# Optimization experiments

Measured on AMD Instinct MI355X. Metric: run time of the kernel, lower is better.

Reference implementation:

```python
import jax, jax.numpy as jnp
import numpy as np

B, S, D, H = 1, 2048, 1024, 16
HD = D // H
S_SLOPE = 10.0      # soft_thres_layer s
C_MASK = -10000.0   # soft_thres_layer c == masked_bias
ALPHA = 0.0         # config.threshold
W_STD = 0.02        # GPT2 init std for weights


def setup_inputs() -> dict:
    key = jax.random.key(0)
    k1, k2, k3 = jax.random.split(key, 3)
    return {
        "hidden_states": jax.random.normal(k1, (B, S, D), dtype=jnp.float32),
        "c_attn_w": jax.random.normal(k2, (D, 3 * D), dtype=jnp.float32) * W_STD,
        "c_attn_b": jnp.zeros((3 * D,), dtype=jnp.float32),
        "c_proj_w": jax.random.normal(k3, (D, D), dtype=jnp.float32) * W_STD,
        "c_proj_b": jnp.zeros((D,), dtype=jnp.float32),
    }


def reference(hidden_states, c_attn_w, c_attn_b, c_proj_w, c_proj_b):
    # Conv1D: x @ w + b (GPT2 convention: weight is [in, out])
    qkv = hidden_states @ c_attn_w + c_attn_b            # [B,S,3D]
    q, k, v = jnp.split(qkv, 3, axis=-1)

    def split_heads(x):
        return x.reshape(B, S, H, HD).transpose(0, 2, 1, 3)  # [B,H,S,hd]

    q, k, v = split_heads(q), split_heads(k), split_heads(v)

    # prun path: NO 1/sqrt(d) scaling (skipped when self.prun is True)
    w = jnp.einsum("bhqd,bhkd->bhqk", q, k)              # [B,H,S,S]

    causal = jnp.tril(jnp.ones((S, S), dtype=bool))[None, None]
    w = jnp.where(causal, w, C_MASK)

    # soft-threshold pruning: smoothly pushes scores below alpha toward c=-10000
    w = C_MASK + (w - C_MASK) * jax.nn.sigmoid(S_SLOPE * (w - ALPHA))

    a = jax.nn.softmax(w, axis=-1)                        # attn_dropout = identity (eval)
    out = jnp.einsum("bhqk,bhkd->bhqd", a, v)             # [B,H,S,hd]
    out = out.transpose(0, 2, 1, 3).reshape(B, S, D)      # merge heads
    return out @ c_proj_w + c_proj_b                      # resid_dropout = identity
```

## Files before the change

kernel.cpp:

```cpp
#include <hip/hip_runtime.h>


#define S_LEN 2048
#define DM    1024
#define NH    16
#define HD    64
#define NQKV  3072
#define SLOPE 10.0f
#define CMASK -10000.0f

typedef short s16x4 __attribute__((ext_vector_type(4)));
typedef short s16x8 __attribute__((ext_vector_type(8)));
typedef float f32x4 __attribute__((ext_vector_type(4)));

#define MFMA16(a,b,c) __builtin_amdgcn_mfma_f32_16x16x32_bf16(a,b,c,0,0,0)
#define GLDS16(g,l) __builtin_amdgcn_global_load_lds( \
    (const __attribute__((address_space(1))) void*)(g), \
    (__attribute__((address_space(3))) void*)(l), 16, 0, 0)

__device__ __forceinline__ short f2bf(float f){
    unsigned u = __float_as_uint(f);
    u += 0x7fffu + ((u >> 16) & 1u);
    return (short)(u >> 16);
}
__device__ __forceinline__ float bf2f(short x){
    return __uint_as_float(((unsigned)(unsigned short)x) << 16);
}
struct bfpair { short hi, lo; };
__device__ __forceinline__ bfpair split_bf(float x){
    bfpair r; r.hi = f2bf(x);
    r.lo = f2bf(x - bf2f(r.hi));
    return r;
}

template<int ROWS, int THREADS>
__device__ __forceinline__ void stage_tile(const short* gbase, int rstride,
                                           short* lds, int tid){
#pragma unroll
    for (int it = 0; it < ROWS*8/THREADS; ++it){
        int s = it*THREADS + tid;
        int row = s >> 3, grp = s & 7;
        const short* src = gbase + (size_t)row*rstride + ((grp ^ (row & 7)) << 3);
        GLDS16(src, lds + (size_t)s*8);
    }
}
__device__ __forceinline__ s16x8 frag(const short* lds, int row, int kg){
    return *(const s16x8*)&lds[row*64 + ((kg ^ (row & 7)) << 3)];
}

template<bool WSPLIT, bool QKV>
__global__ __launch_bounds__(256)
void gemm_kern(const short* __restrict__ Ahg, const short* __restrict__ Alg,
               const short* __restrict__ Bhg, const short* __restrict__ Blg,
               const float* __restrict__ bias,
               short* __restrict__ o0h, short* __restrict__ o0l,
               short* __restrict__ o1h,
               short* __restrict__ o2,  float* __restrict__ oproj)
{
    __shared__ __align__(16) short Ah_s[128*64];
    __shared__ __align__(16) short Al_s[128*64];
    __shared__ __align__(16) short Bh_s[128*64];
    __shared__ __align__(16) short Bl_s[WSPLIT ? 128*64 : 8];

    const int tid = threadIdx.x, lane = tid & 63, wid = tid >> 6;
    const int lr = lane & 15, lg = lane >> 4;
    const int brow = blockIdx.y*128, bcol = blockIdx.x*128;
    const int wm = (wid >> 1)*64, wn = (wid & 1)*64;

    f32x4 acc[4][4];
#pragma unroll
    for (int m = 0; m < 4; ++m)
#pragma unroll
        for (int n = 0; n < 4; ++n) acc[m][n] = (f32x4){0.f,0.f,0.f,0.f};

    for (int k0 = 0; k0 < DM; k0 += 64){
        stage_tile<128,256>(Ahg + (size_t)brow*DM + k0, DM, Ah_s, tid);
        stage_tile<128,256>(Alg + (size_t)brow*DM + k0, DM, Al_s, tid);
        stage_tile<128,256>(Bhg + (size_t)bcol*DM + k0, DM, Bh_s, tid);
        if constexpr (WSPLIT)
            stage_tile<128,256>(Blg + (size_t)bcol*DM + k0, DM, Bl_s, tid);
        __syncthreads();
#pragma unroll
        for (int kc = 0; kc < 2; ++kc){
            s16x8 ah[4], al[4], bh[4], bl[4];
#pragma unroll
            for (int m = 0; m < 4; ++m){
                ah[m] = frag(Ah_s, wm + m*16 + lr, kc*4 + lg);
                al[m] = frag(Al_s, wm + m*16 + lr, kc*4 + lg);
            }
#pragma unroll
            for (int n = 0; n < 4; ++n){
                bh[n] = frag(Bh_s, wn + n*16 + lr, kc*4 + lg);
                if constexpr (WSPLIT)
                    bl[n] = frag(Bl_s, wn + n*16 + lr, kc*4 + lg);
            }
#pragma unroll
            for (int m = 0; m < 4; ++m)
#pragma unroll
                for (int n = 0; n < 4; ++n){
                    acc[m][n] = MFMA16(ah[m], bh[n], acc[m][n]);
                    if constexpr (WSPLIT)
                        acc[m][n] = MFMA16(ah[m], bl[n], acc[m][n]);
                    acc[m][n] = MFMA16(al[m], bh[n], acc[m][n]);
                }
        }
        __syncthreads();
    }

    const int sec = bcol >> 10;
#pragma unroll
    for (int m = 0; m < 4; ++m)
#pragma unroll
        for (int n = 0; n < 4; ++n){
            int row  = brow + wm + m*16 + lg*4;
            int gcol = bcol + wn + n*16 + lr;
            float bv = bias[gcol];
#pragma unroll
            for (int v = 0; v < 4; ++v){
                float val = acc[m][n][v] + bv;
                if constexpr (QKV){
                    int col1 = gcol & 1023;
                    size_t o = (size_t)(row + v)*DM + col1;
                    if (sec == 0){ bfpair p = split_bf(val); o0h[o] = p.hi; o0l[o] = p.lo; }
                    else if (sec == 1){ o1h[o] = f2bf(val); }
                    else { o2[o] = f2bf(val); }
                } else {
                    oproj[(size_t)(row + v)*DM + gcol] = val;
                }
            }
        }
}

__global__ __launch_bounds__(256)
void split_f32(const float* __restrict__ x, short* __restrict__ h,
               short* __restrict__ l, int n4)
{
    int i = blockIdx.x*256 + threadIdx.x;
    if (i >= n4) return;
    float4 v = *(const float4*)&x[(size_t)i*4];
    bfpair a = split_bf(v.x), b = split_bf(v.y), c = split_bf(v.z), d = split_bf(v.w);
    s16x4 hv, lv;
    hv.x = a.hi; hv.y = b.hi; hv.z = c.hi; hv.w = d.hi;
    lv.x = a.lo; lv.y = b.lo; lv.z = c.lo; lv.w = d.lo;
    *(s16x4*)&h[(size_t)i*4] = hv;
    *(s16x4*)&l[(size_t)i*4] = lv;
}

template<bool SPL>
__global__ __launch_bounds__(256)
void wtrans(const float* __restrict__ W, int N, short* __restrict__ Th,
            short* __restrict__ Tl)
{
    __shared__ float t[64][65];
    const int tid = threadIdx.x;
    const int tn = blockIdx.x*64, tk = blockIdx.y*64;
#pragma unroll
    for (int it = 0; it < 4; ++it){
        int idx = tid + it*256;
        int r = idx >> 4, c4 = (idx & 15)*4;
        float4 v = *(const float4*)&W[(size_t)(tk + r)*N + tn + c4];
        t[r][c4] = v.x; t[r][c4+1] = v.y; t[r][c4+2] = v.z; t[r][c4+3] = v.w;
    }
    __syncthreads();
#pragma unroll
    for (int it = 0; it < 4; ++it){
        int idx = tid + it*256;
        int n = idx >> 4, c4 = (idx & 15)*4;
        s16x4 hv, lv;
#pragma unroll
        for (int j = 0; j < 4; ++j){
            bfpair p = split_bf(t[c4+j][n]);
            hv[j] = p.hi; lv[j] = p.lo;
        }
        *(s16x4*)&Th[(size_t)(tn + n)*DM + tk + c4] = hv;
        if constexpr (SPL) *(s16x4*)&Tl[(size_t)(tn + n)*DM + tk + c4] = lv;
    }
}

__global__ __launch_bounds__(256)
void vtrans(const short* __restrict__ Vb, short* __restrict__ Vt)
{
    __shared__ short t[64][66];
    const int tid = threadIdx.x;
    const int td = blockIdx.x*64, ts = blockIdx.y*64;
#pragma unroll
    for (int it = 0; it < 4; ++it){
        int idx = tid + it*256;
        int r = idx >> 4, c4 = (idx & 15)*4;
        s16x4 v = *(const s16x4*)&Vb[(size_t)(ts + r)*DM + td + c4];
        t[r][c4] = v.x; t[r][c4+1] = v.y; t[r][c4+2] = v.z; t[r][c4+3] = v.w;
    }
    __syncthreads();
#pragma unroll
    for (int it = 0; it < 4; ++it){
        int idx = tid + it*256;
        int n = idx >> 4, c4 = (idx & 15)*4;
        s16x4 o;
#pragma unroll
        for (int j = 0; j < 4; ++j) o[j] = t[c4+j][n];
        *(s16x4*)&Vt[(size_t)(td + n)*S_LEN + ts + c4] = o;
    }
}

__global__ __launch_bounds__(64)
void sv_partial(const short* __restrict__ Vb, float* __restrict__ PB)
{
    int b = blockIdx.x, h = blockIdx.y, d = threadIdx.x;
    float s = 0.f;
#pragma unroll 8
    for (int k = 0; k < 64; ++k)
        s += bf2f(Vb[(size_t)(b*64 + k)*DM + h*HD + d]);
    PB[((size_t)h*32 + b)*64 + d] = s;
}
__global__ __launch_bounds__(64)
void sv_suffix(const float* __restrict__ PB, float* __restrict__ SSV)
{
    int h = blockIdx.x, d = threadIdx.x;
    float s = 0.f;
    SSV[((size_t)h*33 + 32)*64 + d] = 0.f;
    for (int b = 31; b >= 0; --b){
        s += PB[((size_t)h*32 + b)*64 + d];
        SSV[((size_t)h*33 + b)*64 + d] = s;
    }
}

__global__ __launch_bounds__(64)
void attn_fwd(const short* __restrict__ Qh, const short* __restrict__ Ql,
              const short* __restrict__ Kh, const short* __restrict__ Vt,
              const float* __restrict__ SSV,
              short* __restrict__ Oh, short* __restrict__ Ol)
{
    __shared__ __align__(16) short Ps[16*72];

    const int id = blockIdx.x;
    const int h  = (id & 7) + 8*((id >> 3) & 1);
    const int qt = 127 - (id >> 4);
    const int diag = qt >> 2;

    const int lane = threadIdx.x, lr = lane & 15, lg = lane >> 4;
    const int qrow = qt*16 + lg*4;

    const short* qbh = Qh + (size_t)(qt*16)*DM + h*HD;
    const short* qbl = Ql + (size_t)(qt*16)*DM + h*HD;
    s16x8 aqh[2], aql[2];
#pragma unroll
    for (int kc = 0; kc < 2; ++kc){
        aqh[kc] = *(const s16x8*)&qbh[(size_t)lr*DM + kc*32 + lg*8];
        aql[kc] = *(const s16x8*)&qbl[(size_t)lr*DM + kc*32 + lg*8];
    }

    float m_run[4], l_run[4];
    f32x4 acc_o[4];
#pragma unroll
    for (int v = 0; v < 4; ++v){ m_run[v] = -1e30f; l_run[v] = 0.f; }
#pragma unroll
    for (int n = 0; n < 4; ++n) acc_o[n] = (f32x4){0.f,0.f,0.f,0.f};

    const short* kb0 = Kh + (size_t)h*HD;
    const short* vb0 = Vt + (size_t)(h*HD)*S_LEN;

    for (int kvb = 0; kvb <= diag; ++kvb){
        const short* kb = kb0 + (size_t)(kvb*64)*DM;
        s16x8 bk[2][4];
#pragma unroll
        for (int kc = 0; kc < 2; ++kc)
#pragma unroll
            for (int n = 0; n < 4; ++n)
                bk[kc][n] = *(const s16x8*)&kb[(size_t)(n*16 + lr)*DM + kc*32 + lg*8];

        f32x4 sc[4];
#pragma unroll
        for (int n = 0; n < 4; ++n) sc[n] = (f32x4){0.f,0.f,0.f,0.f};
#pragma unroll
        for (int kc = 0; kc < 2; ++kc)
#pragma unroll
            for (int n = 0; n < 4; ++n){
                sc[n] = MFMA16(aqh[kc], bk[kc][n], sc[n]);
                sc[n] = MFMA16(aql[kc], bk[kc][n], sc[n]);
            }

        const short* vb = vb0 + kvb*64;
        s16x8 bv0[4], bv1[4];
#pragma unroll
        for (int n = 0; n < 4; ++n){
            bv0[n] = *(const s16x8*)&vb[(size_t)(16*n + lr)*S_LEN + lg*8];
            bv1[n] = *(const s16x8*)&vb[(size_t)(16*n + lr)*S_LEN + 32 + lg*8];
        }

        float p[4][4], tmax[4];
#pragma unroll
        for (int v = 0; v < 4; ++v) tmax[v] = -1e30f;
        if (kvb == diag){
#pragma unroll
            for (int n = 0; n < 4; ++n){
                int key = kvb*64 + n*16 + lr;
#pragma unroll
                for (int v = 0; v < 4; ++v){
                    float w;
                    if (key > qrow + v) w = CMASK;
                    else {
                        float sv = sc[n][v];
                        float sig = 1.f / (1.f + __expf(-SLOPE*sv));
                        w = CMASK + (sv - CMASK)*sig;
                    }
                    p[n][v] = w;
                    tmax[v] = fmaxf(tmax[v], w);
                }
            }
        } else {
#pragma unroll
            for (int n = 0; n < 4; ++n)
#pragma unroll
                for (int v = 0; v < 4; ++v){
                    float sv = sc[n][v];
                    float sig = 1.f / (1.f + __expf(-SLOPE*sv));
                    float w = CMASK + (sv - CMASK)*sig;
                    p[n][v] = w;
                    tmax[v] = fmaxf(tmax[v], w);
                }
        }
#pragma unroll
        for (int v = 0; v < 4; ++v)
#pragma unroll
            for (int msk = 1; msk < 16; msk <<= 1)
                tmax[v] = fmaxf(tmax[v], __shfl_xor(tmax[v], msk, 64));

        float scale[4], rsum[4];
#pragma unroll
        for (int v = 0; v < 4; ++v){
            float mn = fmaxf(m_run[v], tmax[v]);
            scale[v] = __expf(m_run[v] - mn);
            m_run[v] = mn;
            rsum[v] = 0.f;
        }
#pragma unroll
        for (int n = 0; n < 4; ++n)
#pragma unroll
            for (int v = 0; v < 4; ++v){
                float e = __expf(p[n][v] - m_run[v]);
                p[n][v] = e;
                rsum[v] += e;
            }
#pragma unroll
        for (int v = 0; v < 4; ++v){
#pragma unroll
            for (int msk = 1; msk < 16; msk <<= 1)
                rsum[v] += __shfl_xor(rsum[v], msk, 64);
            l_run[v] = l_run[v]*scale[v] + rsum[v];
        }
#pragma unroll
        for (int n = 0; n < 4; ++n)
#pragma unroll
            for (int v = 0; v < 4; ++v) acc_o[n][v] *= scale[v];

#pragma unroll
        for (int n = 0; n < 4; ++n)
#pragma unroll
            for (int v = 0; v < 4; ++v)
                Ps[(lg*4 + v)*72 + 16*n + lr] = f2bf(p[n][v]);
        asm volatile("s_waitcnt lgkmcnt(0)" ::: "memory");

        s16x8 pa0 = *(const s16x8*)&Ps[lr*72 + lg*8];
        s16x8 pa1 = *(const s16x8*)&Ps[lr*72 + 32 + lg*8];
#pragma unroll
        for (int n = 0; n < 4; ++n){
            acc_o[n] = MFMA16(pa0, bv0[n], acc_o[n]);
            acc_o[n] = MFMA16(pa1, bv1[n], acc_o[n]);
        }
    }

    {
        const float* sv = SSV + ((size_t)h*33 + (diag + 1))*64;
        float F = (float)(S_LEN - 64*(diag + 1));
        float e[4];
#pragma unroll
        for (int v = 0; v < 4; ++v){
            e[v] = __expf(CMASK - m_run[v]);
            l_run[v] += e[v]*F;
        }
#pragma unroll
        for (int n = 0; n < 4; ++n){
            float svv = sv[16*n + lr];
#pragma unroll
            for (int v = 0; v < 4; ++v) acc_o[n][v] += e[v]*svv;
        }
    }

#pragma unroll
    for (int n = 0; n < 4; ++n)
#pragma unroll
        for (int v = 0; v < 4; ++v){
            int row = qt*16 + lg*4 + v;
            int col = h*HD + 16*n + lr;
            bfpair p = split_bf(acc_o[n][v] / l_run[v]);
            Oh[(size_t)row*DM + col] = p.hi;
            Ol[(size_t)row*DM + col] = p.lo;
        }
}

extern "C" void kernel_launch(void* const* d_in, const int* in_sizes, int n_in,
                              void* d_out, int out_size, void* d_ws, size_t ws_size,
                              hipStream_t stream)
{
    (void)in_sizes; (void)n_in; (void)out_size; (void)ws_size;
    const float* hs   = (const float*)d_in[0];
    const float* wqkv = (const float*)d_in[1];
    const float* bqkv = (const float*)d_in[2];
    const float* wprj = (const float*)d_in[3];
    const float* bprj = (const float*)d_in[4];

    char* p = (char*)d_ws;
    short* Ahg  = (short*)(p + (0ull  << 20));
    short* Alg  = (short*)(p + (4ull  << 20));
    short* WqTh = (short*)(p + (8ull  << 20));
    short* WqTl = (short*)(p + (14ull << 20));
    short* Qhg  = (short*)(p + (20ull << 20));
    short* Qlg  = (short*)(p + (24ull << 20));
    short* Khg  = (short*)(p + (28ull << 20));
    short* Vbg  = (short*)(p + (32ull << 20));
    short* Vtg  = (short*)(p + (36ull << 20));
    float* PB   = (float*)(p + (40ull << 20));
    float* SSV  = (float*)(p + (41ull << 20));
    short* Oh = Ahg, * Ol = Alg;
    short* WpT = WqTh;

    split_f32<<<S_LEN*DM/4/256, 256, 0, stream>>>(hs, Ahg, Alg, S_LEN*DM/4);
    wtrans<true><<<dim3(NQKV/64, DM/64), 256, 0, stream>>>(wqkv, NQKV, WqTh, WqTl);

    gemm_kern<true, true><<<dim3(NQKV/128, S_LEN/128), 256, 0, stream>>>(
        Ahg, Alg, WqTh, WqTl, bqkv, Qhg, Qlg, Khg, Vbg, nullptr);

    wtrans<false><<<dim3(DM/64, DM/64), 256, 0, stream>>>(wprj, DM, WpT, nullptr);
    vtrans<<<dim3(DM/64, S_LEN/64), 256, 0, stream>>>(Vbg, Vtg);
    sv_partial<<<dim3(32, NH), 64, 0, stream>>>(Vbg, PB);
    sv_suffix<<<NH, 64, 0, stream>>>(PB, SSV);

    attn_fwd<<<2048, 64, 0, stream>>>(Qhg, Qlg, Khg, Vtg, SSV, Oh, Ol);

    gemm_kern<false, false><<<dim3(DM/128, S_LEN/128), 256, 0, stream>>>(
        Oh, Ol, WpT, nullptr, bprj, nullptr, nullptr, nullptr, nullptr,
        (float*)d_out);
}
```

Baseline: 173.3 us.

## Write V transposed from QKV GEMM, fuse sum kernels, split attention across two waves

The QKV GEMM epilogue now writes V directly in transposed layout, which removes the separate vtrans kernel. The two V suffix-sum kernels are merged into one sv_kern that reads the transposed V. The attention kernel goes from one wave to two per block: each wave takes alternating KV blocks and prefetches the next K tile, and the two partial online-softmax states are merged through shared memory at the end. The aim is fewer launches and less memory traffic, plus more parallelism per query tile. The costs are strided 8-byte stores in the GEMM epilogue, a serial 16-block sv_kern that reads each row in a long loop, and extra registers and LDS in attention.

```diff
diff --git a/kernel.cpp b/kernel.cpp
--- a/kernel.cpp
+++ b/kernel.cpp
@@ -55,7 +55,7 @@
                const float* __restrict__ bias,
                short* __restrict__ o0h, short* __restrict__ o0l,
                short* __restrict__ o1h,
-               short* __restrict__ o2,  float* __restrict__ oproj)
+               short* __restrict__ oVt, float* __restrict__ oproj)
 {
     __shared__ __align__(16) short Ah_s[128*64];
     __shared__ __align__(16) short Al_s[128*64];
@@ -115,17 +115,24 @@
             int row  = brow + wm + m*16 + lg*4;
             int gcol = bcol + wn + n*16 + lr;
             float bv = bias[gcol];
-#pragma unroll
-            for (int v = 0; v < 4; ++v){
-                float val = acc[m][n][v] + bv;
-                if constexpr (QKV){
-                    int col1 = gcol & 1023;
-                    size_t o = (size_t)(row + v)*DM + col1;
-                    if (sec == 0){ bfpair p = split_bf(val); o0h[o] = p.hi; o0l[o] = p.lo; }
-                    else if (sec == 1){ o1h[o] = f2bf(val); }
-                    else { o2[o] = f2bf(val); }
-                } else {
-                    oproj[(size_t)(row + v)*DM + gcol] = val;
+            if (QKV && sec == 2){
+                int col1 = gcol & 1023;
+                s16x4 vv;
+#pragma unroll
+                for (int v = 0; v < 4; ++v) vv[v] = f2bf(acc[m][n][v] + bv);
+                *(s16x4*)&oVt[(size_t)col1*S_LEN + row] = vv;
+            } else {
+#pragma unroll
+                for (int v = 0; v < 4; ++v){
+                    float val = acc[m][n][v] + bv;
+                    if constexpr (QKV){
+                        int col1 = gcol & 1023;
+                        size_t o = (size_t)(row + v)*DM + col1;
+                        if (sec == 0){ bfpair p = split_bf(val); o0h[o] = p.hi; o0l[o] = p.lo; }
+                        else { o1h[o] = f2bf(val); }
+                    } else {
+                        oproj[(size_t)(row + v)*DM + gcol] = val;
+                    }
                 }
             }
         }
@@ -177,67 +184,38 @@
     }
 }
 
-__global__ __launch_bounds__(256)
-void vtrans(const short* __restrict__ Vb, short* __restrict__ Vt)
-{
-    __shared__ short t[64][66];
-    const int tid = threadIdx.x;
-    const int td = blockIdx.x*64, ts = blockIdx.y*64;
-#pragma unroll
-    for (int it = 0; it < 4; ++it){
-        int idx = tid + it*256;
-        int r = idx >> 4, c4 = (idx & 15)*4;
-        s16x4 v = *(const s16x4*)&Vb[(size_t)(ts + r)*DM + td + c4];
-        t[r][c4] = v.x; t[r][c4+1] = v.y; t[r][c4+2] = v.z; t[r][c4+3] = v.w;
-    }
-    __syncthreads();
-#pragma unroll
-    for (int it = 0; it < 4; ++it){
-        int idx = tid + it*256;
-        int n = idx >> 4, c4 = (idx & 15)*4;
-        s16x4 o;
-#pragma unroll
-        for (int j = 0; j < 4; ++j) o[j] = t[c4+j][n];
-        *(s16x4*)&Vt[(size_t)(td + n)*S_LEN + ts + c4] = o;
-    }
-}
-
 __global__ __launch_bounds__(64)
-void sv_partial(const short* __restrict__ Vb, float* __restrict__ PB)
-{
-    int b = blockIdx.x, h = blockIdx.y, d = threadIdx.x;
-    float s = 0.f;
-#pragma unroll 8
-    for (int k = 0; k < 64; ++k)
-        s += bf2f(Vb[(size_t)(b*64 + k)*DM + h*HD + d]);
-    PB[((size_t)h*32 + b)*64 + d] = s;
-}
-__global__ __launch_bounds__(64)
-void sv_suffix(const float* __restrict__ PB, float* __restrict__ SSV)
+void sv_kern(const short* __restrict__ Vt, float* __restrict__ SSV)
 {
     int h = blockIdx.x, d = threadIdx.x;
+    const short* row = Vt + (size_t)(h*HD + d)*S_LEN;
     float s = 0.f;
     SSV[((size_t)h*33 + 32)*64 + d] = 0.f;
     for (int b = 31; b >= 0; --b){
-        s += PB[((size_t)h*32 + b)*64 + d];
+        float bs = 0.f;
+#pragma unroll 8
+        for (int k = 0; k < 64; ++k) bs += bf2f(row[b*64 + k]);
+        s += bs;
         SSV[((size_t)h*33 + b)*64 + d] = s;
     }
 }
 
-__global__ __launch_bounds__(64)
+__global__ __launch_bounds__(128)
 void attn_fwd(const short* __restrict__ Qh, const short* __restrict__ Ql,
               const short* __restrict__ Kh, const short* __restrict__ Vt,
               const float* __restrict__ SSV,
               short* __restrict__ Oh, short* __restrict__ Ol)
 {
-    __shared__ __align__(16) short Ps[16*72];
+    __shared__ __align__(16) short Ps[2][16*72];
+    __shared__ float mrg[64][26];
 
     const int id = blockIdx.x;
     const int h  = (id & 7) + 8*((id >> 3) & 1);
     const int qt = 127 - (id >> 4);
     const int diag = qt >> 2;
 
-    const int lane = threadIdx.x, lr = lane & 15, lg = lane >> 4;
+    const int tid = threadIdx.x, lane = tid & 63, wid = tid >> 6;
+    const int lr = lane & 15, lg = lane >> 4;
     const int qrow = qt*16 + lg*4;
 
     const short* qbh = Qh + (size_t)(qt*16)*DM + h*HD;
@@ -259,14 +237,26 @@
     const short* kb0 = Kh + (size_t)h*HD;
     const short* vb0 = Vt + (size_t)(h*HD)*S_LEN;
 
-    for (int kvb = 0; kvb <= diag; ++kvb){
-        const short* kb = kb0 + (size_t)(kvb*64)*DM;
-        s16x8 bk[2][4];
+    s16x8 bkc[2][4];
+    if (wid <= diag){
+        const short* kb = kb0 + (size_t)(wid*64)*DM;
 #pragma unroll
         for (int kc = 0; kc < 2; ++kc)
 #pragma unroll
             for (int n = 0; n < 4; ++n)
-                bk[kc][n] = *(const s16x8*)&kb[(size_t)(n*16 + lr)*DM + kc*32 + lg*8];
+                bkc[kc][n] = *(const s16x8*)&kb[(size_t)(n*16 + lr)*DM + kc*32 + lg*8];
+    }
+
+    for (int kvb = wid; kvb <= diag; kvb += 2){
+        s16x8 bkn[2][4];
+        if (kvb + 2 <= diag){
+            const short* kb = kb0 + (size_t)((kvb+2)*64)*DM;
+#pragma unroll
+            for (int kc = 0; kc < 2; ++kc)
+#pragma unroll
+                for (int n = 0; n < 4; ++n)
+                    bkn[kc][n] = *(const s16x8*)&kb[(size_t)(n*16 + lr)*DM + kc*32 + lg*8];
+        }
 
         f32x4 sc[4];
 #pragma unroll
@@ -275,8 +265,8 @@
         for (int kc = 0; kc < 2; ++kc)
 #pragma unroll
             for (int n = 0; n < 4; ++n){
-                sc[n] = MFMA16(aqh[kc], bk[kc][n], sc[n]);
-                sc[n] = MFMA16(aql[kc], bk[kc][n], sc[n]);
+                sc[n] = MFMA16(aqh[kc], bkc[kc][n], sc[n]);
+                sc[n] = MFMA16(aql[kc], bkc[kc][n], sc[n]);
             }
 
         const short* vb = vb0 + kvb*64;
@@ -357,17 +347,53 @@
         for (int n = 0; n < 4; ++n)
 #pragma unroll
             for (int v = 0; v < 4; ++v)
-                Ps[(lg*4 + v)*72 + 16*n + lr] = f2bf(p[n][v]);
+                Ps[wid][(lg*4 + v)*72 + 16*n + lr] = f2bf(p[n][v]);
         asm volatile("s_waitcnt lgkmcnt(0)" ::: "memory");
 
-        s16x8 pa0 = *(const s16x8*)&Ps[lr*72 + lg*8];
-        s16x8 pa1 = *(const s16x8*)&Ps[lr*72 + 32 + lg*8];
+        s16x8 pa0 = *(const s16x8*)&Ps[wid][lr*72 + lg*8];
+        s16x8 pa1 = *(const s16x8*)&Ps[wid][lr*72 + 32 + lg*8];
 #pragma unroll
         for (int n = 0; n < 4; ++n){
             acc_o[n] = MFMA16(pa0, bv0[n], acc_o[n]);
             acc_o[n] = MFMA16(pa1, bv1[n], acc_o[n]);
         }
-    }
+
+#pragma unroll
+        for (int kc = 0; kc < 2; ++kc)
+#pragma unroll
+            for (int n = 0; n < 4; ++n) bkc[kc][n] = bkn[kc][n];
+    }
+
+    if (wid == 1){
+#pragma unroll
+        for (int v = 0; v < 4; ++v){
+            mrg[lane][v] = m_run[v];
+            mrg[lane][4 + v] = l_run[v];
+        }
+#pragma unroll
+        for (int n = 0; n < 4; ++n)
+#pragma unroll
+            for (int v = 0; v < 4; ++v) mrg[lane][8 + n*4 + v] = acc_o[n][v];
+    }
+    __syncthreads();
+    if (wid != 0) return;
+
+    float e0[4];
+#pragma unroll
+    for (int v = 0; v < 4; ++v){
+        float m1 = mrg[lane][v], l1 = mrg[lane][4 + v];
+        float mn = fmaxf(m_run[v], m1);
+        e0[v] = __expf(m_run[v] - mn);
+        float e1 = __expf(m1 - mn);
+        l_run[v] = l_run[v]*e0[v] + l1*e1;
+        m_run[v] = mn;
+        mrg[lane][4 + v] = e1;
+    }
+#pragma unroll
+    for (int n = 0; n < 4; ++n)
+#pragma unroll
+        for (int v = 0; v < 4; ++v)
+            acc_o[n][v] = acc_o[n][v]*e0[v] + mrg[lane][8 + n*4 + v]*mrg[lane][4 + v];
 
     {
         const float* sv = SSV + ((size_t)h*33 + (diag + 1))*64;
@@ -417,25 +443,23 @@
     short* Qhg  = (short*)(p + (20ull << 20));
     short* Qlg  = (short*)(p + (24ull << 20));
     short* Khg  = (short*)(p + (28ull << 20));
-    short* Vbg  = (short*)(p + (32ull << 20));
-    short* Vtg  = (short*)(p + (36ull << 20));
-    float* PB   = (float*)(p + (40ull << 20));
-    float* SSV  = (float*)(p + (41ull << 20));
+    short* Vtg  = (short*)(p + (32ull << 20));
+    float* PB   = (float*)(p + (36ull << 20));
+    float* SSV  = (float*)(p + (37ull << 20));
     short* Oh = Ahg, * Ol = Alg;
     short* WpT = WqTh;
+    (void)PB;
 
     split_f32<<<S_LEN*DM/4/256, 256, 0, stream>>>(hs, Ahg, Alg, S_LEN*DM/4);
     wtrans<true><<<dim3(NQKV/64, DM/64), 256, 0, stream>>>(wqkv, NQKV, WqTh, WqTl);
 
     gemm_kern<true, true><<<dim3(NQKV/128, S_LEN/128), 256, 0, stream>>>(
-        Ahg, Alg, WqTh, WqTl, bqkv, Qhg, Qlg, Khg, Vbg, nullptr);
+        Ahg, Alg, WqTh, WqTl, bqkv, Qhg, Qlg, Khg, Vtg, nullptr);
 
     wtrans<false><<<dim3(DM/64, DM/64), 256, 0, stream>>>(wprj, DM, WpT, nullptr);
-    vtrans<<<dim3(DM/64, S_LEN/64), 256, 0, stream>>>(Vbg, Vtg);
-    sv_partial<<<dim3(32, NH), 64, 0, stream>>>(Vbg, PB);
-    sv_suffix<<<NH, 64, 0, stream>>>(PB, SSV);
-
-    attn_fwd<<<2048, 64, 0, stream>>>(Qhg, Qlg, Khg, Vtg, SSV, Oh, Ol);
+    sv_kern<<<NH, 64, 0, stream>>>(Vtg, SSV);
+
+    attn_fwd<<<2048, 128, 0, stream>>>(Qhg, Qlg, Khg, Vtg, SSV, Oh, Ol);
 
     gemm_kern<false, false><<<dim3(DM/128, S_LEN/128), 256, 0, stream>>>(
         Oh, Ol, WpT, nullptr, bprj, nullptr, nullptr, nullptr, nullptr,
```

New measurement: 196.2 us. 13.2% more time.

## Split attention KV loop across four waves with LDS merge and K prefetch

Applied to the files above, without the earlier changes.

Each attention block now runs four wavefronts. They stride over the key/value blocks of one 16-row query tile, so the serial KV loop per tile becomes about four times shorter. Each wave keeps its own running max, sum and output accumulator, and wave 0 merges the partial softmax states through shared memory after a barrier. The K fragments for the next iteration are also prefetched into registers. This cuts the long serial latency chain on diagonal-heavy tiles, at the cost of more registers, extra LDS traffic, a merge step, and idle waves on short tiles.

```diff
diff --git a/kernel.cpp b/kernel.cpp
--- a/kernel.cpp
+++ b/kernel.cpp
@@ -224,20 +224,22 @@
     }
 }
 
-__global__ __launch_bounds__(64)
+__global__ __launch_bounds__(256)
 void attn_fwd(const short* __restrict__ Qh, const short* __restrict__ Ql,
               const short* __restrict__ Kh, const short* __restrict__ Vt,
               const float* __restrict__ SSV,
               short* __restrict__ Oh, short* __restrict__ Ol)
 {
-    __shared__ __align__(16) short Ps[16*72];
+    __shared__ __align__(16) short Ps[4][16*72];
+    __shared__ float mrg[3][64][24];
 
     const int id = blockIdx.x;
     const int h  = (id & 7) + 8*((id >> 3) & 1);
     const int qt = 127 - (id >> 4);
     const int diag = qt >> 2;
 
-    const int lane = threadIdx.x, lr = lane & 15, lg = lane >> 4;
+    const int tid = threadIdx.x, lane = tid & 63, wid = tid >> 6;
+    const int lr = lane & 15, lg = lane >> 4;
     const int qrow = qt*16 + lg*4;
 
     const short* qbh = Qh + (size_t)(qt*16)*DM + h*HD;
@@ -259,14 +261,26 @@
     const short* kb0 = Kh + (size_t)h*HD;
     const short* vb0 = Vt + (size_t)(h*HD)*S_LEN;
 
-    for (int kvb = 0; kvb <= diag; ++kvb){
-        const short* kb = kb0 + (size_t)(kvb*64)*DM;
-        s16x8 bk[2][4];
+    s16x8 bkc[2][4];
+    if (wid <= diag){
+        const short* kb = kb0 + (size_t)(wid*64)*DM;
 #pragma unroll
         for (int kc = 0; kc < 2; ++kc)
 #pragma unroll
             for (int n = 0; n < 4; ++n)
-                bk[kc][n] = *(const s16x8*)&kb[(size_t)(n*16 + lr)*DM + kc*32 + lg*8];
+                bkc[kc][n] = *(const s16x8*)&kb[(size_t)(n*16 + lr)*DM + kc*32 + lg*8];
+    }
+
+    for (int kvb = wid; kvb <= diag; kvb += 4){
+        s16x8 bkn[2][4];
+        if (kvb + 4 <= diag){
+            const short* kb = kb0 + (size_t)((kvb+4)*64)*DM;
+#pragma unroll
+            for (int kc = 0; kc < 2; ++kc)
+#pragma unroll
+                for (int n = 0; n < 4; ++n)
+                    bkn[kc][n] = *(const s16x8*)&kb[(size_t)(n*16 + lr)*DM + kc*32 + lg*8];
+        }
 
         f32x4 sc[4];
 #pragma unroll
@@ -275,8 +289,8 @@
         for (int kc = 0; kc < 2; ++kc)
 #pragma unroll
             for (int n = 0; n < 4; ++n){
-                sc[n] = MFMA16(aqh[kc], bk[kc][n], sc[n]);
-                sc[n] = MFMA16(aql[kc], bk[kc][n], sc[n]);
+                sc[n] = MFMA16(aqh[kc], bkc[kc][n], sc[n]);
+                sc[n] = MFMA16(aql[kc], bkc[kc][n], sc[n]);
             }
 
         const short* vb = vb0 + kvb*64;
@@ -357,16 +371,54 @@
         for (int n = 0; n < 4; ++n)
 #pragma unroll
             for (int v = 0; v < 4; ++v)
-                Ps[(lg*4 + v)*72 + 16*n + lr] = f2bf(p[n][v]);
+                Ps[wid][(lg*4 + v)*72 + 16*n + lr] = f2bf(p[n][v]);
         asm volatile("s_waitcnt lgkmcnt(0)" ::: "memory");
 
-        s16x8 pa0 = *(const s16x8*)&Ps[lr*72 + lg*8];
-        s16x8 pa1 = *(const s16x8*)&Ps[lr*72 + 32 + lg*8];
+        s16x8 pa0 = *(const s16x8*)&Ps[wid][lr*72 + lg*8];
+        s16x8 pa1 = *(const s16x8*)&Ps[wid][lr*72 + 32 + lg*8];
 #pragma unroll
         for (int n = 0; n < 4; ++n){
             acc_o[n] = MFMA16(pa0, bv0[n], acc_o[n]);
             acc_o[n] = MFMA16(pa1, bv1[n], acc_o[n]);
         }
+
+#pragma unroll
+        for (int kc = 0; kc < 2; ++kc)
+#pragma unroll
+            for (int n = 0; n < 4; ++n) bkc[kc][n] = bkn[kc][n];
+    }
+
+    if (wid != 0){
+#pragma unroll
+        for (int v = 0; v < 4; ++v){
+            mrg[wid-1][lane][v] = m_run[v];
+            mrg[wid-1][lane][4 + v] = l_run[v];
+        }
+#pragma unroll
+        for (int n = 0; n < 4; ++n)
+#pragma unroll
+            for (int v = 0; v < 4; ++v) mrg[wid-1][lane][8 + n*4 + v] = acc_o[n][v];
+    }
+    __syncthreads();
+    if (wid != 0) return;
+
+#pragma unroll
+    for (int w = 0; w < 3; ++w){
+        float e0[4], e1[4];
+#pragma unroll
+        for (int v = 0; v < 4; ++v){
+            float m1 = mrg[w][lane][v], l1 = mrg[w][lane][4 + v];
+            float mn = fmaxf(m_run[v], m1);
+            e0[v] = __expf(m_run[v] - mn);
+            e1[v] = __expf(m1 - mn);
+            l_run[v] = l_run[v]*e0[v] + l1*e1[v];
+            m_run[v] = mn;
+        }
+#pragma unroll
+        for (int n = 0; n < 4; ++n)
+#pragma unroll
+            for (int v = 0; v < 4; ++v)
+                acc_o[n][v] = acc_o[n][v]*e0[v] + mrg[w][lane][8 + n*4 + v]*e1[v];
     }
 
     {
@@ -435,7 +487,7 @@
     sv_partial<<<dim3(32, NH), 64, 0, stream>>>(Vbg, PB);
     sv_suffix<<<NH, 64, 0, stream>>>(PB, SSV);
 
-    attn_fwd<<<2048, 64, 0, stream>>>(Qhg, Qlg, Khg, Vtg, SSV, Oh, Ol);
+    attn_fwd<<<2048, 256, 0, stream>>>(Qhg, Qlg, Khg, Vtg, SSV, Oh, Ol);
 
     gemm_kern<false, false><<<dim3(DM/128, S_LEN/128), 256, 0, stream>>>(
         Oh, Ol, WpT, nullptr, bprj, nullptr, nullptr, nullptr, nullptr,
```

Result: faster. 169.8 us (-2.0%).
